# Kernel tuning notes

Measured on AMD Instinct MI355X. Metric: run time of the kernel, lower is better.

Reference implementation:

```python
import jax, jax.numpy as jnp
import numpy as np

NEG = -1e30

def setup_inputs() -> dict:
    key = jax.random.key(0)
    k1, k2, k3, k4, k5, k6, k7, k8 = jax.random.split(key, 8)
    B, Ti, Tm = 4, 512, 1024
    Din, Dmem, D = 256, 256, 64
    inputs = jax.random.normal(k1, (B, Ti, Din), dtype=jnp.float32)
    memory = jax.random.normal(k2, (B, Tm, Dmem), dtype=jnp.float32)
    input_lengths = jax.random.randint(k3, (B,), 1, Ti + 1)
    memory_lengths = jax.random.randint(k4, (B,), 1, Tm + 1)
    s_in = 1.0 / np.sqrt(Din)
    s_d = 1.0 / np.sqrt(D)
    W_in = jax.random.uniform(k5, (D, Din), jnp.float32, -s_in, s_in)
    b_in = jax.random.uniform(k6, (D,), jnp.float32, -s_in, s_in)
    W_mem = jax.random.uniform(k7, (D, Dmem), jnp.float32, -s_in, s_in)
    W_final = jax.random.uniform(k8, (D,), jnp.float32, -s_d, s_d)
    return {"inputs": inputs, "memory": memory,
            "input_lengths": input_lengths, "memory_lengths": memory_lengths,
            "W_in": W_in, "b_in": b_in, "W_mem": W_mem, "W_final": W_final}

def reference(inputs, memory, input_lengths, memory_lengths, W_in, b_in, W_mem, W_final):
    # inputs: (B,Ti,Din), memory: (B,Tm,Dmem)
    input_item = jnp.einsum('bid,td->bit', inputs, W_in) + b_in      # (B,Ti,D)
    memory_item = jnp.einsum('bmd,td->bmt', memory, W_mem)           # (B,Tm,D)
    items = jnp.tanh(input_item[:, :, None, :] + memory_item[:, None, :, :])  # (B,Ti,Tm,D)
    score = jnp.einsum('bitd,d->bit'.replace('t', 'mt')[:0] or 'bimd,d->bim', items, W_final)  # (B,Ti,Tm)
    Ti = inputs.shape[-2]
    Tm = memory.shape[-2]
    in_mask = jnp.arange(Ti)[None, :] < input_lengths[:, None]       # (B,Ti)
    mem_mask = jnp.arange(Tm)[None, :] < memory_lengths[:, None]     # (B,Tm)
    score = jnp.where(in_mask[:, :, None], score, NEG)
    score = jnp.where(mem_mask[:, None, :], score, NEG)
    attn = jax.nn.softmax(score, axis=-1)                            # (B,Ti,Tm)
    out = jnp.einsum('bim,bmd->bid', attn, memory)                   # (B,Ti,Dmem)
    return out
```

## Files before the change

### kernel.cpp

```cpp
#include <hip/hip_runtime.h>

__device__ __forceinline__ float fast_tanh(float x) {
  float e = __expf(2.0f * x);
  return 1.0f - 2.0f * __builtin_amdgcn_rcpf(e + 1.0f);
}

__global__ __launch_bounds__(256) void proj_kernel(
    const float* __restrict__ inputs, const float* __restrict__ memory,
    const float* __restrict__ W_in, const float* __restrict__ b_in,
    const float* __restrict__ W_mem,
    float* __restrict__ in_item, float* __restrict__ mem_item)
{
  const int NIN = 2048;
  int r0 = blockIdx.x * 16;
  int tid = threadIdx.x;
  __shared__ float4 wlds[64][64];

  const float* Wsel; const float* Abase; float* O; int ar0; bool has_bias = (r0 < NIN);
  if (has_bias) { Wsel = W_in;  Abase = inputs; O = in_item;  ar0 = r0; }
  else          { Wsel = W_mem; Abase = memory; O = mem_item; ar0 = r0 - NIN; }

  const float4* Wv = reinterpret_cast<const float4*>(Wsel);
  #pragma unroll
  for (int u = 0; u < 16; ++u) {
    int e = tid + u * 256;
    int k4 = e & 63, dd = e >> 6;
    wlds[k4][dd ^ (k4 & 7)] = Wv[e];
  }
  int d = tid & 63, rg = tid >> 6;
  float bias = has_bias ? b_in[d] : 0.f;
  __syncthreads();

  const float4* A0 = reinterpret_cast<const float4*>(Abase + (size_t)(ar0 + rg) * 256);
  float acc0 = 0.f, acc1 = 0.f, acc2 = 0.f, acc3 = 0.f;
  #pragma unroll 8
  for (int k4 = 0; k4 < 64; ++k4) {
    float4 w  = wlds[k4][d ^ (k4 & 7)];
    float4 a0 = A0[k4];
    float4 a1 = A0[k4 + 256];
    float4 a2 = A0[k4 + 512];
    float4 a3 = A0[k4 + 768];
    acc0 += a0.x*w.x + a0.y*w.y + a0.z*w.z + a0.w*w.w;
    acc1 += a1.x*w.x + a1.y*w.y + a1.z*w.z + a1.w*w.w;
    acc2 += a2.x*w.x + a2.y*w.y + a2.z*w.z + a2.w*w.w;
    acc3 += a3.x*w.x + a3.y*w.y + a3.z*w.z + a3.w*w.w;
  }
  O[(size_t)(ar0 + rg     ) * 64 + d] = acc0 + bias;
  O[(size_t)(ar0 + rg +  4) * 64 + d] = acc1 + bias;
  O[(size_t)(ar0 + rg +  8) * 64 + d] = acc2 + bias;
  O[(size_t)(ar0 + rg + 12) * 64 + d] = acc3 + bias;
}

__global__ __launch_bounds__(512, 4) void attn_kernel(
    const float* __restrict__ in_item,
    const float* __restrict__ mem_item,
    const float* __restrict__ memory,
    const int* __restrict__ in_len, const int* __restrict__ mem_len,
    const float* __restrict__ W_final,
    float* __restrict__ out)
{
  const int Ti = 512, Tm = 1024, DM = 256;
  const int TI = 4, MT = 128, NT = Tm / MT;
  int b = blockIdx.y;
  int i0 = blockIdx.x * TI;
  int tid = threadIdx.x;

  __shared__ float4 mt4[16][MT];
  __shared__ float4 pt4[MT];
  __shared__ float  q[TI][64];
  __shared__ float  wf[64];
  __shared__ float4 oacc4[TI][64];
  __shared__ float  red[8];
  __shared__ float  inv_s[TI];

  if (tid < TI * 64) {
    int ii = tid >> 6, dd = tid & 63;
    q[ii][dd] = in_item[((size_t)b * Ti + i0 + ii) * 64 + dd];
  } else if (tid < TI * 64 + 64) {
    wf[tid - TI * 64] = W_final[tid - TI * 64];
  }
  if (tid < TI * 64) {
    oacc4[tid >> 6][tid & 63] = make_float4(0.f, 0.f, 0.f, 0.f);
  }
  int ilen = in_len[b], mlen = mem_len[b];

  const int s_ii = tid >> 7, s_ml = tid & 127;
  const bool row_valid = (i0 + s_ii) < ilen;
  float psum = 0.f;

  const int dq = tid & 63, chunk = tid >> 6;
  float4 a0 = make_float4(0,0,0,0), a1 = a0, a2 = a0, a3 = a0;
  const float* memb = memory + (size_t)b * Tm * DM;

  for (int t = 0; t < NT; ++t) {
    int m0 = t * MT;
    __syncthreads();

    #pragma unroll
    for (int u = 0; u < 4; ++u) {
      int e = tid + u * 512;
      int dd4 = e & 15, mm = e >> 4;
      float4 v = reinterpret_cast<const float4*>(mem_item)[((size_t)b * Tm + m0 + mm) * 16 + dd4];
      mt4[dd4][mm ^ (dd4 & 7)] = v;
    }
    __syncthreads();

    {
      const float4* qq = reinterpret_cast<const float4*>(q[s_ii]);
      const float4* ww = reinterpret_cast<const float4*>(wf);
      float sc = 0.f;
      #pragma unroll
      for (int d4 = 0; d4 < 16; ++d4) {
        float4 mv = mt4[d4][s_ml ^ (d4 & 7)];
        float4 qv = qq[d4];
        float4 wv = ww[d4];
        sc += fast_tanh(qv.x + mv.x) * wv.x
            + fast_tanh(qv.y + mv.y) * wv.y
            + fast_tanh(qv.z + mv.z) * wv.z
            + fast_tanh(qv.w + mv.w) * wv.w;
      }
      int m = m0 + s_ml;
      float p = row_valid ? ((m < mlen) ? __expf(sc) : 0.f) : 1.0f;
      reinterpret_cast<float*>(&pt4[s_ml])[s_ii] = p;
      psum += p;
    }
    __syncthreads();

    {
      const float* mpb = memb + (size_t)(m0 + chunk * 16) * DM + dq * 4;
      #pragma unroll
      for (int mm = 0; mm < 16; ++mm) {
        float4 v = *reinterpret_cast<const float4*>(mpb + (size_t)mm * DM);
        float4 p = pt4[chunk * 16 + mm];
        a0.x += p.x*v.x; a0.y += p.x*v.y; a0.z += p.x*v.z; a0.w += p.x*v.w;
        a1.x += p.y*v.x; a1.y += p.y*v.y; a1.z += p.y*v.z; a1.w += p.y*v.w;
        a2.x += p.z*v.x; a2.y += p.z*v.y; a2.z += p.z*v.z; a2.w += p.z*v.w;
        a3.x += p.w*v.x; a3.y += p.w*v.y; a3.z += p.w*v.z; a3.w += p.w*v.w;
      }
    }
  }
  __syncthreads();

  {
    float s = psum;
    #pragma unroll
    for (int o = 32; o >= 1; o >>= 1) s += __shfl_xor(s, o);
    if ((tid & 63) == 0) red[tid >> 6] = s;
  }
  __syncthreads();
  if (tid < TI) inv_s[tid] = 1.0f / (red[2 * tid] + red[2 * tid + 1]);

  for (int ph = 0; ph < 8; ++ph) {
    if (chunk == ph) {
      float4 t0 = oacc4[0][dq]; t0.x+=a0.x; t0.y+=a0.y; t0.z+=a0.z; t0.w+=a0.w; oacc4[0][dq]=t0;
      float4 t1 = oacc4[1][dq]; t1.x+=a1.x; t1.y+=a1.y; t1.z+=a1.z; t1.w+=a1.w; oacc4[1][dq]=t1;
      float4 t2 = oacc4[2][dq]; t2.x+=a2.x; t2.y+=a2.y; t2.z+=a2.z; t2.w+=a2.w; oacc4[2][dq]=t2;
      float4 t3 = oacc4[3][dq]; t3.x+=a3.x; t3.y+=a3.y; t3.z+=a3.z; t3.w+=a3.w; oacc4[3][dq]=t3;
    }
    __syncthreads();
  }

  #pragma unroll
  for (int u = 0; u < 2; ++u) {
    int e = tid + u * 512;
    int ii = e >> 8, dd = e & 255;
    float val = reinterpret_cast<const float*>(oacc4[ii])[dd] * inv_s[ii];
    out[((size_t)b * Ti + i0 + ii) * DM + dd] = val;
  }
}

extern "C" void kernel_launch(void* const* d_in, const int* in_sizes, int n_in,
                              void* d_out, int out_size, void* d_ws, size_t ws_size,
                              hipStream_t stream) {
  const float* inputs   = (const float*)d_in[0];
  const float* memory   = (const float*)d_in[1];
  const int*   in_len   = (const int*)  d_in[2];
  const int*   mem_len  = (const int*)  d_in[3];
  const float* W_in     = (const float*)d_in[4];
  const float* b_in     = (const float*)d_in[5];
  const float* W_mem    = (const float*)d_in[6];
  const float* W_final  = (const float*)d_in[7];
  float* out = (float*)d_out;

  float* in_item  = (float*)d_ws;
  float* mem_item = in_item + 2048 * 64;

  proj_kernel<<<384, 256, 0, stream>>>(inputs, memory, W_in, b_in, W_mem,
                                       in_item, mem_item);
  attn_kernel<<<dim3(128, 4), 512, 0, stream>>>(in_item, mem_item, memory,
                                                in_len, mem_len, W_final, out);
}
```

Baseline: 85.80 us.

## Fold tanh constants into projections, restructure score loop and final reduction

Pre-scales the projected items by 2*log2(e) so the tanh reduces to exp2 plus reciprocal. The sum over W_final*tanh is rewritten as Wsum - 2*sum(w*sigmoid-like), and both the constant and the exp are folded into a single exp2 fma. The query row now lives in registers instead of LDS. Barriers drop from three to two per tile by loading the next mem_item tile after the score phase. The serialized 8-phase accumulation becomes a parallel LDS tree reduction with vectorized float4 stores. The exp2 of sums can overflow to inf, which rcp maps to 0, so it should still be correct, though the numerics differ slightly.

```diff
diff --git a/kernel.cpp b/kernel.cpp
--- a/kernel.cpp
+++ b/kernel.cpp
@@ -1,9 +1,7 @@
 #include <hip/hip_runtime.h>
 
-__device__ __forceinline__ float fast_tanh(float x) {
-  float e = __expf(2.0f * x);
-  return 1.0f - 2.0f * __builtin_amdgcn_rcpf(e + 1.0f);
-}
+#define C2  2.8853900817779268f
+#define L2E 1.4426950408889634f
 
 __global__ __launch_bounds__(256) void proj_kernel(
     const float* __restrict__ inputs, const float* __restrict__ memory,
@@ -45,10 +43,10 @@
     acc2 += a2.x*w.x + a2.y*w.y + a2.z*w.z + a2.w*w.w;
     acc3 += a3.x*w.x + a3.y*w.y + a3.z*w.z + a3.w*w.w;
   }
-  O[(size_t)(ar0 + rg     ) * 64 + d] = acc0 + bias;
-  O[(size_t)(ar0 + rg +  4) * 64 + d] = acc1 + bias;
-  O[(size_t)(ar0 + rg +  8) * 64 + d] = acc2 + bias;
-  O[(size_t)(ar0 + rg + 12) * 64 + d] = acc3 + bias;
+  O[(size_t)(ar0 + rg     ) * 64 + d] = (acc0 + bias) * C2;
+  O[(size_t)(ar0 + rg +  4) * 64 + d] = (acc1 + bias) * C2;
+  O[(size_t)(ar0 + rg +  8) * 64 + d] = (acc2 + bias) * C2;
+  O[(size_t)(ar0 + rg + 12) * 64 + d] = (acc3 + bias) * C2;
 }
 
 __global__ __launch_bounds__(512, 4) void attn_kernel(
@@ -60,112 +58,119 @@
     float* __restrict__ out)
 {
   const int Ti = 512, Tm = 1024, DM = 256;
-  const int TI = 4, MT = 128, NT = Tm / MT;
+  const int TI = 4, MT = 128, NT = 8;
   int b = blockIdx.y;
   int i0 = blockIdx.x * TI;
   int tid = threadIdx.x;
 
-  __shared__ float4 mt4[16][MT];
-  __shared__ float4 pt4[MT];
-  __shared__ float  q[TI][64];
-  __shared__ float  wf[64];
-  __shared__ float4 oacc4[TI][64];
+  __shared__ float4 smem[16 * 128];
+  __shared__ float4 pt4[128];
   __shared__ float  red[8];
-  __shared__ float  inv_s[TI];
 
-  if (tid < TI * 64) {
-    int ii = tid >> 6, dd = tid & 63;
-    q[ii][dd] = in_item[((size_t)b * Ti + i0 + ii) * 64 + dd];
-  } else if (tid < TI * 64 + 64) {
-    wf[tid - TI * 64] = W_final[tid - TI * 64];
+  const int s_ii = __builtin_amdgcn_readfirstlane(tid >> 7);
+  const int s_ml = tid & 127;
+  const int dq = tid & 63, wv_ = tid >> 6;
+
+  float4 qreg[16];
+  {
+    const float4* qrow = reinterpret_cast<const float4*>(
+        in_item + ((size_t)b * Ti + i0 + s_ii) * 64);
+    #pragma unroll
+    for (int j = 0; j < 16; ++j) qreg[j] = qrow[j];
   }
-  if (tid < TI * 64) {
-    oacc4[tid >> 6][tid & 63] = make_float4(0.f, 0.f, 0.f, 0.f);
-  }
+
+  float Wsum = 0.f;
+  #pragma unroll
+  for (int j = 0; j < 64; ++j) Wsum += W_final[j];
+  const float c1 = L2E * Wsum;
+  const float4* Wf4 = reinterpret_cast<const float4*>(W_final);
+
   int ilen = in_len[b], mlen = mem_len[b];
+  const bool row_valid = (i0 + s_ii) < ilen;
 
-  const int s_ii = tid >> 7, s_ml = tid & 127;
-  const bool row_valid = (i0 + s_ii) < ilen;
-  float psum = 0.f;
-
-  const int dq = tid & 63, chunk = tid >> 6;
-  float4 a0 = make_float4(0,0,0,0), a1 = a0, a2 = a0, a3 = a0;
+  const float4* mem4 = reinterpret_cast<const float4*>(mem_item);
   const float* memb = memory + (size_t)b * Tm * DM;
 
+  float psum = 0.f;
+  float4 a0 = make_float4(0,0,0,0), a1 = a0, a2 = a0, a3 = a0;
+
+  #pragma unroll
+  for (int u = 0; u < 4; ++u) {
+    int e = tid + u * 512, dd4 = e & 15, mm = e >> 4;
+    smem[dd4 * 128 + (mm ^ (dd4 & 7))] = mem4[((size_t)b * Tm + mm) * 16 + dd4];
+  }
+  __syncthreads();
+
+  #pragma unroll 1
   for (int t = 0; t < NT; ++t) {
     int m0 = t * MT;
+
+    float4 S4 = make_float4(0,0,0,0);
+    #pragma unroll
+    for (int d4 = 0; d4 < 16; ++d4) {
+      float4 mv = smem[d4 * 128 + (s_ml ^ (d4 & 7))];
+      float4 qv = qreg[d4];
+      float4 w  = Wf4[d4];
+      S4.x = fmaf(w.x, __builtin_amdgcn_rcpf(1.0f + __builtin_amdgcn_exp2f(qv.x + mv.x)), S4.x);
+      S4.y = fmaf(w.y, __builtin_amdgcn_rcpf(1.0f + __builtin_amdgcn_exp2f(qv.y + mv.y)), S4.y);
+      S4.z = fmaf(w.z, __builtin_amdgcn_rcpf(1.0f + __builtin_amdgcn_exp2f(qv.z + mv.z)), S4.z);
+      S4.w = fmaf(w.w, __builtin_amdgcn_rcpf(1.0f + __builtin_amdgcn_exp2f(qv.w + mv.w)), S4.w);
+    }
+    float S = (S4.x + S4.y) + (S4.z + S4.w);
+    int m = m0 + s_ml;
+    float p = row_valid ? ((m < mlen) ? __builtin_amdgcn_exp2f(fmaf(-C2, S, c1)) : 0.f)
+                        : 1.0f;
+    reinterpret_cast<float*>(&pt4[s_ml])[s_ii] = p;
+    psum += p;
     __syncthreads();
 
-    #pragma unroll
-    for (int u = 0; u < 4; ++u) {
-      int e = tid + u * 512;
-      int dd4 = e & 15, mm = e >> 4;
-      float4 v = reinterpret_cast<const float4*>(mem_item)[((size_t)b * Tm + m0 + mm) * 16 + dd4];
-      mt4[dd4][mm ^ (dd4 & 7)] = v;
+    if (t + 1 < NT) {
+      int m0n = m0 + MT;
+      #pragma unroll
+      for (int u = 0; u < 4; ++u) {
+        int e = tid + u * 512, dd4 = e & 15, mm = e >> 4;
+        smem[dd4 * 128 + (mm ^ (dd4 & 7))] = mem4[((size_t)b * Tm + m0n + mm) * 16 + dd4];
+      }
     }
-    __syncthreads();
 
     {
-      const float4* qq = reinterpret_cast<const float4*>(q[s_ii]);
-      const float4* ww = reinterpret_cast<const float4*>(wf);
-      float sc = 0.f;
-      #pragma unroll
-      for (int d4 = 0; d4 < 16; ++d4) {
-        float4 mv = mt4[d4][s_ml ^ (d4 & 7)];
-        float4 qv = qq[d4];
-        float4 wv = ww[d4];
-        sc += fast_tanh(qv.x + mv.x) * wv.x
-            + fast_tanh(qv.y + mv.y) * wv.y
-            + fast_tanh(qv.z + mv.z) * wv.z
-            + fast_tanh(qv.w + mv.w) * wv.w;
-      }
-      int m = m0 + s_ml;
-      float p = row_valid ? ((m < mlen) ? __expf(sc) : 0.f) : 1.0f;
-      reinterpret_cast<float*>(&pt4[s_ml])[s_ii] = p;
-      psum += p;
-    }
-    __syncthreads();
-
-    {
-      const float* mpb = memb + (size_t)(m0 + chunk * 16) * DM + dq * 4;
+      const float* mpb = memb + (size_t)(m0 + wv_ * 16) * DM + dq * 4;
       #pragma unroll
       for (int mm = 0; mm < 16; ++mm) {
         float4 v = *reinterpret_cast<const float4*>(mpb + (size_t)mm * DM);
-        float4 p = pt4[chunk * 16 + mm];
-        a0.x += p.x*v.x; a0.y += p.x*v.y; a0.z += p.x*v.z; a0.w += p.x*v.w;
-        a1.x += p.y*v.x; a1.y += p.y*v.y; a1.z += p.y*v.z; a1.w += p.y*v.w;
-        a2.x += p.z*v.x; a2.y += p.z*v.y; a2.z += p.z*v.z; a2.w += p.z*v.w;
-        a3.x += p.w*v.x; a3.y += p.w*v.y; a3.z += p.w*v.z; a3.w += p.w*v.w;
+        float4 pp = pt4[wv_ * 16 + mm];
+        a0.x += pp.x*v.x; a0.y += pp.x*v.y; a0.z += pp.x*v.z; a0.w += pp.x*v.w;
+        a1.x += pp.y*v.x; a1.y += pp.y*v.y; a1.z += pp.y*v.z; a1.w += pp.y*v.w;
+        a2.x += pp.z*v.x; a2.y += pp.z*v.y; a2.z += pp.z*v.z; a2.w += pp.z*v.w;
+        a3.x += pp.w*v.x; a3.y += pp.w*v.y; a3.z += pp.w*v.z; a3.w += pp.w*v.w;
       }
     }
+    __syncthreads();
   }
-  __syncthreads();
 
   {
     float s = psum;
     #pragma unroll
     for (int o = 32; o >= 1; o >>= 1) s += __shfl_xor(s, o);
-    if ((tid & 63) == 0) red[tid >> 6] = s;
+    if (dq == 0) red[wv_] = s;
   }
+  smem[(wv_ * 4 + 0) * 64 + dq] = a0;
+  smem[(wv_ * 4 + 1) * 64 + dq] = a1;
+  smem[(wv_ * 4 + 2) * 64 + dq] = a2;
+  smem[(wv_ * 4 + 3) * 64 + dq] = a3;
   __syncthreads();
-  if (tid < TI) inv_s[tid] = 1.0f / (red[2 * tid] + red[2 * tid + 1]);
 
-  for (int ph = 0; ph < 8; ++ph) {
-    if (chunk == ph) {
-      float4 t0 = oacc4[0][dq]; t0.x+=a0.x; t0.y+=a0.y; t0.z+=a0.z; t0.w+=a0.w; oacc4[0][dq]=t0;
-      float4 t1 = oacc4[1][dq]; t1.x+=a1.x; t1.y+=a1.y; t1.z+=a1.z; t1.w+=a1.w; oacc4[1][dq]=t1;
-      float4 t2 = oacc4[2][dq]; t2.x+=a2.x; t2.y+=a2.y; t2.z+=a2.z; t2.w+=a2.w; oacc4[2][dq]=t2;
-      float4 t3 = oacc4[3][dq]; t3.x+=a3.x; t3.y+=a3.y; t3.z+=a3.z; t3.w+=a3.w; oacc4[3][dq]=t3;
+  if (tid < 256) {
+    int ii = tid >> 6, d2 = tid & 63;
+    float4 s = smem[ii * 64 + d2];
+    #pragma unroll
+    for (int w = 1; w < 8; ++w) {
+      float4 v = smem[(w * 4 + ii) * 64 + d2];
+      s.x += v.x; s.y += v.y; s.z += v.z; s.w += v.w;
     }
-    __syncthreads();
-  }
-
-  #pragma unroll
-  for (int u = 0; u < 2; ++u) {
-    int e = tid + u * 512;
-    int ii = e >> 8, dd = e & 255;
-    float val = reinterpret_cast<const float*>(oacc4[ii])[dd] * inv_s[ii];
-    out[((size_t)b * Ti + i0 + ii) * DM + dd] = val;
+    float inv = __builtin_amdgcn_rcpf(red[2 * ii] + red[2 * ii + 1]);
+    s.x *= inv; s.y *= inv; s.z *= inv; s.w *= inv;
+    reinterpret_cast<float4*>(out)[((size_t)b * Ti + i0 + ii) * 64 + d2] = s;
   }
 }
 
```

Result: faster. 74.41 us (-13.3%).
